# Kernel optimization log

Hardware: AMD Instinct MI355X
Metric: run time of the kernel (lower is better)

Reference implementation:

```python
import math
import jax, jax.numpy as jnp
import numpy as np

B, C, H, W = 8, 512, 32, 32
NUM_HEADS = 8
HEAD_DIM = C // NUM_HEADS


def setup_inputs() -> dict:
    key = jax.random.key(0)
    ks = jax.random.split(key, 5)
    scale = 1.0 / math.sqrt(C)
    return {
        "x": jax.random.normal(ks[0], (B, C, H, W), dtype=jnp.float32),
        "Wq": jax.random.normal(ks[1], (C, C), dtype=jnp.float32) * scale,
        "bq": jnp.zeros((C,), dtype=jnp.float32),
        "Wk": jax.random.normal(ks[2], (C, C), dtype=jnp.float32) * scale,
        "bk": jnp.zeros((C,), dtype=jnp.float32),
        "Wv": jax.random.normal(ks[3], (C, C), dtype=jnp.float32) * scale,
        "bv": jnp.zeros((C,), dtype=jnp.float32),
        "Wo": jax.random.normal(ks[4], (C, C), dtype=jnp.float32) * scale,
        "bo": jnp.zeros((C,), dtype=jnp.float32),
    }


def reference(x, Wq, bq, Wk, bk, Wv, bv, Wo, bo):
    b, c, h, w = x.shape
    t = h * w
    # (B,C,H,W) -> (B,T,C) token sequence
    xt = x.reshape(b, c, t).transpose(0, 2, 1)
    Q = xt @ Wq + bq
    K = xt @ Wk + bk
    V = xt @ Wv + bv
    # (B,T,C) -> (B,nh,T,hd)
    def split_heads(z):
        return z.reshape(b, t, NUM_HEADS, HEAD_DIM).transpose(0, 2, 1, 3)
    Qh, Kh, Vh = split_heads(Q), split_heads(K), split_heads(V)
    S = jnp.einsum("bhqd,bhkd->bhqk", Qh, Kh) / math.sqrt(HEAD_DIM)
    A = jax.nn.softmax(S, axis=-1)  # dropout p=0.0 -> identity
    Y = jnp.einsum("bhqk,bhkd->bhqd", A, Vh)
    Y = Y.transpose(0, 2, 1, 3).reshape(b, t, c)
    O = Y @ Wo + bo
    out = xt + O
    return out.transpose(0, 2, 1).reshape(b, c, h, w)
```

## Files before the change

### kernel.cpp

```cpp
#include <hip/hip_runtime.h>
#include <hip/hip_bf16.h>

#define B_  8
#define C_  512
#define T_  1024
#define NH_ 8
#define HD_ 64

using short8 = __attribute__((ext_vector_type(8))) short;
using f32x4  = __attribute__((ext_vector_type(4))) float;
using us4    = __attribute__((ext_vector_type(4))) unsigned short;
using u32x2  = __attribute__((ext_vector_type(2))) unsigned int;

__device__ __forceinline__ unsigned short f2bf(float f) {
    unsigned u = __builtin_bit_cast(unsigned, f);
    u += 0x7fff + ((u >> 16) & 1);
    return (unsigned short)(u >> 16);
}
__device__ __forceinline__ unsigned pack2bf(float lo, float hi) {
    __hip_bfloat162 h = __float22bfloat162_rn(float2{lo, hi});
    unsigned u;
    __builtin_memcpy(&u, &h, 4);
    return u;
}

__device__ __forceinline__ void gload_lds16(const ushort* g, ushort* l) {
    __builtin_amdgcn_global_load_lds(
        (const __attribute__((address_space(1))) void*)g,
        (__attribute__((address_space(3))) void*)l, 16, 0, 0);
}

__global__ __launch_bounds__(256) void k_transpose_x(const float* __restrict__ x,
                                                     ushort* __restrict__ xt) {
    __shared__ float tile[32][33];
    int b = blockIdx.z, t0 = blockIdx.x * 32, c0 = blockIdx.y * 32;
    int tx = threadIdx.x & 31, ty = threadIdx.x >> 5;
#pragma unroll
    for (int i = 0; i < 4; i++)
        tile[ty + i * 8][tx] = x[((size_t)b * C_ + c0 + ty + i * 8) * T_ + t0 + tx];
    __syncthreads();
#pragma unroll
    for (int i = 0; i < 4; i++)
        xt[((size_t)b * T_ + t0 + ty + i * 8) * C_ + c0 + tx] = f2bf(tile[tx][ty + i * 8]);
}

__global__ __launch_bounds__(256) void k_transpose_w(const float* __restrict__ Wq,
                                                     const float* __restrict__ Wk,
                                                     const float* __restrict__ Wv,
                                                     const float* __restrict__ Wo,
                                                     ushort* __restrict__ Wqkvt,
                                                     ushort* __restrict__ Wot) {
    __shared__ float tile[32][33];
    int m = blockIdx.z;
    const float* W = (m == 0) ? Wq : (m == 1) ? Wk : (m == 2) ? Wv : Wo;
    ushort* dst = (m < 3) ? (Wqkvt + (size_t)m * C_ * C_) : Wot;
    float scale = (m == 0) ? 0.125f : 1.0f;
    int k0 = blockIdx.x * 32, n0 = blockIdx.y * 32;
    int tx = threadIdx.x & 31, ty = threadIdx.x >> 5;
#pragma unroll
    for (int i = 0; i < 4; i++)
        tile[ty + i * 8][tx] = W[(size_t)(k0 + ty + i * 8) * C_ + n0 + tx];
    __syncthreads();
#pragma unroll
    for (int i = 0; i < 4; i++)
        dst[(size_t)(n0 + ty + i * 8) * C_ + k0 + tx] = f2bf(tile[tx][ty + i * 8] * scale);
}

__device__ __forceinline__ void gemm_core(const ushort* __restrict__ A,
                                          const ushort* __restrict__ Bt,
                                          int row0, int col0, int tid,
                                          ushort* As, ushort* Bs, f32x4 acc[4][4]) {
    f32x4 zero = {0.f, 0.f, 0.f, 0.f};
#pragma unroll
    for (int i = 0; i < 4; i++)
#pragma unroll
        for (int j = 0; j < 4; j++) acc[i][j] = zero;
    int lane = tid & 63, w = tid >> 6;
    int ql = lane & 15, g = lane >> 4;
    int wm = (w >> 1) * 64, wn = (w & 1) * 64;
    int srow = lane >> 3;
    int scol8 = (lane & 7) ^ (srow & 7);

    for (int k0 = 0; k0 < C_; k0 += 64) {
#pragma unroll
        for (int i = 0; i < 4; i++) {
            int c = w * 4 + i;
            int r = c * 8 + srow;
            gload_lds16(A + (size_t)(row0 + r) * C_ + k0 + scol8 * 8, As + c * 512);
            gload_lds16(Bt + (size_t)(col0 + r) * C_ + k0 + scol8 * 8, Bs + c * 512);
        }
        __syncthreads();
#pragma unroll
        for (int s = 0; s < 2; s++) {
            short8 a[4], b[4];
            int cs = ((4 * s + g) ^ (ql & 7)) * 8;
#pragma unroll
            for (int mt = 0; mt < 4; mt++)
                a[mt] = *(const short8*)(As + (wm + mt * 16 + ql) * 64 + cs);
#pragma unroll
            for (int nt = 0; nt < 4; nt++)
                b[nt] = *(const short8*)(Bs + (wn + nt * 16 + ql) * 64 + cs);
#pragma unroll
            for (int mt = 0; mt < 4; mt++)
#pragma unroll
                for (int nt = 0; nt < 4; nt++)
                    acc[mt][nt] = __builtin_amdgcn_mfma_f32_16x16x32_bf16(
                        a[mt], b[nt], acc[mt][nt], 0, 0, 0);
        }
        __syncthreads();
    }
}

__global__ __launch_bounds__(256) void k_qkv(const ushort* __restrict__ xt,
                                             const ushort* __restrict__ Wqkvt,
                                             const float* __restrict__ bq,
                                             const float* __restrict__ bk,
                                             const float* __restrict__ bv,
                                             ushort* __restrict__ Qh,
                                             ushort* __restrict__ Kh,
                                             ushort* __restrict__ Vt) {
    __shared__ __align__(16) ushort As[128 * 64];
    __shared__ __align__(16) ushort Bs[128 * 64];
    f32x4 acc[4][4];
    int tid = threadIdx.x;
    int row0 = blockIdx.x * 128, col0 = blockIdx.y * 128;
    gemm_core(xt, Wqkvt, row0, col0, tid, As, Bs, acc);
    int lane = tid & 63, w = tid >> 6;
    int wm = (w >> 1) * 64, wn = (w & 1) * 64;
    int which = col0 >> 9;
    const float* bias = (which == 0) ? bq : (which == 1) ? bk : bv;
    float bscale = (which == 0) ? 0.125f : 1.0f;
#pragma unroll
    for (int mt = 0; mt < 4; mt++) {
        int grow0 = row0 + wm + mt * 16 + ((lane >> 4) << 2);
        int b = grow0 >> 10, t = grow0 & 1023;
#pragma unroll
        for (int nt = 0; nt < 4; nt++) {
            int gcol = col0 + wn + nt * 16 + (lane & 15);
            int hc = gcol & 511;
            float bsv = bias[hc] * bscale;
            int h = hc >> 6, d = hc & 63;
            if (which == 2) {
                us4 pk;
#pragma unroll
                for (int r = 0; r < 4; r++) pk[r] = f2bf(acc[mt][nt][r] + bsv);
                *(us4*)(Vt + ((size_t)(b * NH_ + h) * HD_ + d) * T_ + t) = pk;
            } else {
                ushort* dst = (which == 0) ? Qh : Kh;
#pragma unroll
                for (int r = 0; r < 4; r++)
                    dst[((size_t)(b * NH_ + h) * T_ + t + r) * HD_ + d] =
                        f2bf(acc[mt][nt][r] + bsv);
            }
        }
    }
}

__global__ __launch_bounds__(512) void k_attn(const ushort* __restrict__ Qh,
                                              const ushort* __restrict__ Kh,
                                              const ushort* __restrict__ Vt,
                                              ushort* __restrict__ Y) {
    __shared__ __align__(16) ushort Ks[2][64 * 64];
    __shared__ __align__(16) ushort Vs[2][64 * 64];
    __shared__ __align__(16) ushort Pws[8][16 * 64];
    int tid = threadIdx.x, lane = tid & 63, w = tid >> 6;
    int g = lane >> 4, ql = lane & 15;
    int bh = blockIdx.x & 63, q0 = (blockIdx.x >> 6) * 128;
    int b = bh >> 3, h = bh & 7;
    ushort* Pw = Pws[w];
    int srow = lane >> 3;
    int scol8 = (lane & 7) ^ (srow & 7);
    const ushort* Kbase = Kh + (size_t)bh * T_ * HD_;
    const ushort* Vbase = Vt + (size_t)bh * HD_ * T_;

    short8 qa[2];
#pragma unroll
    for (int s = 0; s < 2; s++)
        qa[s] = *(const short8*)(Qh + ((size_t)bh * T_ + q0 + w * 16 + ql) * HD_ + s * 32 + g * 8);

    short8 ones;
    {
        short ov = (ql == 0) ? (short)0x3F80 : (short)0;
#pragma unroll
        for (int j = 0; j < 8; j++) ones[j] = ov;
    }

    f32x4 o[4], o5;
    f32x4 zero = {0.f, 0.f, 0.f, 0.f};
#pragma unroll
    for (int i = 0; i < 4; i++) o[i] = zero;
    o5 = zero;

    {
        int r = w * 8 + srow;
        gload_lds16(Kbase + (size_t)r * HD_ + scol8 * 8, Ks[0] + w * 512);
        gload_lds16(Vbase + (size_t)r * T_ + scol8 * 8, Vs[0] + w * 512);
    }
    __syncthreads();

    for (int t = 0; t < 16; t++) {
        int cur = t & 1;
        const ushort* Kc = Ks[cur];
        const ushort* Vc = Vs[cur];
        if (t < 15) {
            int kv0 = (t + 1) * 64;
            int r = w * 8 + srow;
            gload_lds16(Kbase + (size_t)(kv0 + r) * HD_ + scol8 * 8, Ks[cur ^ 1] + w * 512);
            gload_lds16(Vbase + (size_t)r * T_ + kv0 + scol8 * 8, Vs[cur ^ 1] + w * 512);
        }

        f32x4 sT[4];
#pragma unroll
        for (int nt = 0; nt < 4; nt++) sT[nt] = zero;
        __builtin_amdgcn_s_setprio(1);
#pragma unroll
        for (int s = 0; s < 2; s++) {
            int cs = ((4 * s + g) ^ (ql & 7)) * 8;
#pragma unroll
            for (int nt = 0; nt < 4; nt++) {
                short8 ka = *(const short8*)(Kc + (nt * 16 + ql) * 64 + cs);
                sT[nt] = __builtin_amdgcn_mfma_f32_16x16x32_bf16(ka, qa[s], sT[nt], 0, 0, 0);
            }
        }
        __builtin_amdgcn_s_setprio(0);

#pragma unroll
        for (int nt = 0; nt < 4; nt++) {
            u32x2 pk;
            pk[0] = pack2bf(__expf(sT[nt][0]), __expf(sT[nt][1]));
            pk[1] = pack2bf(__expf(sT[nt][2]), __expf(sT[nt][3]));
            int gr = (2 * nt + (g >> 1)) ^ (ql & 7);
            *(u32x2*)(Pw + ql * 64 + gr * 8 + (g & 1) * 4) = pk;
        }

        __builtin_amdgcn_s_setprio(1);
#pragma unroll
        for (int s = 0; s < 2; s++) {
            int cs = ((4 * s + g) ^ (ql & 7)) * 8;
            short8 pa = *(const short8*)(Pw + ql * 64 + cs);
#pragma unroll
            for (int dt = 0; dt < 4; dt++) {
                short8 vb = *(const short8*)(Vc + (dt * 16 + ql) * 64 + cs);
                o[dt] = __builtin_amdgcn_mfma_f32_16x16x32_bf16(pa, vb, o[dt], 0, 0, 0);
            }
            o5 = __builtin_amdgcn_mfma_f32_16x16x32_bf16(pa, ones, o5, 0, 0, 0);
        }
        __builtin_amdgcn_s_setprio(0);
        __syncthreads();
    }

    float li[4];
#pragma unroll
    for (int r = 0; r < 4; r++) li[r] = 1.0f / __shfl(o5[r], g * 16);
#pragma unroll
    for (int dt = 0; dt < 4; dt++)
#pragma unroll
        for (int r = 0; r < 4; r++) {
            int t = q0 + w * 16 + 4 * g + r;
            int c = h * HD_ + dt * 16 + ql;
            Y[((size_t)b * T_ + t) * C_ + c] = f2bf(o[dt][r] * li[r]);
        }
}

__global__ __launch_bounds__(256) void k_oproj(const ushort* __restrict__ Y,
                                               const ushort* __restrict__ Wot,
                                               const float* __restrict__ bo,
                                               const float* __restrict__ x,
                                               float* __restrict__ out) {
    __shared__ __align__(16) ushort As[128 * 64];
    __shared__ __align__(16) ushort Bs[128 * 64];
    f32x4 acc[4][4];
    int tid = threadIdx.x;
    int row0 = blockIdx.x * 128, col0 = blockIdx.y * 128;
    gemm_core(Y, Wot, row0, col0, tid, As, Bs, acc);
    int lane = tid & 63, w = tid >> 6;
    int wm = (w >> 1) * 64, wn = (w & 1) * 64;
#pragma unroll
    for (int mt = 0; mt < 4; mt++) {
        int grow0 = row0 + wm + mt * 16 + ((lane >> 4) << 2);
        int b = grow0 >> 10, t = grow0 & 1023;
#pragma unroll
        for (int nt = 0; nt < 4; nt++) {
            int c = col0 + wn + nt * 16 + (lane & 15);
            float bsv = bo[c];
            size_t off = ((size_t)b * C_ + c) * T_ + t;
            float4 xv = *(const float4*)(x + off);
            float4 ov;
            ov.x = acc[mt][nt][0] + xv.x + bsv;
            ov.y = acc[mt][nt][1] + xv.y + bsv;
            ov.z = acc[mt][nt][2] + xv.z + bsv;
            ov.w = acc[mt][nt][3] + xv.w + bsv;
            *(float4*)(out + off) = ov;
        }
    }
}

extern "C" void kernel_launch(void* const* d_in, const int* in_sizes, int n_in,
                              void* d_out, int out_size, void* d_ws, size_t ws_size,
                              hipStream_t stream) {
    const float* x  = (const float*)d_in[0];
    const float* Wq = (const float*)d_in[1];
    const float* bq = (const float*)d_in[2];
    const float* Wk = (const float*)d_in[3];
    const float* bk = (const float*)d_in[4];
    const float* Wv = (const float*)d_in[5];
    const float* bv = (const float*)d_in[6];
    const float* Wo = (const float*)d_in[7];
    const float* bo = (const float*)d_in[8];
    float* out = (float*)d_out;

    char* ws = (char*)d_ws;
    ushort* xt    = (ushort*)(ws + 0);
    ushort* Wqkvt = (ushort*)(ws + 8388608);
    ushort* Wot   = (ushort*)(ws + 9961472);
    ushort* Qh    = (ushort*)(ws + 10485760);
    ushort* Kh    = (ushort*)(ws + 18874368);
    ushort* Vt    = (ushort*)(ws + 27262976);
    ushort* Yw    = xt;

    k_transpose_x<<<dim3(32, 16, 8), 256, 0, stream>>>(x, xt);
    k_transpose_w<<<dim3(16, 16, 4), 256, 0, stream>>>(Wq, Wk, Wv, Wo, Wqkvt, Wot);
    k_qkv<<<dim3(64, 12), 256, 0, stream>>>(xt, Wqkvt, bq, bk, bv, Qh, Kh, Vt);
    k_attn<<<dim3(512), 512, 0, stream>>>(Qh, Kh, Vt, Yw);
    k_oproj<<<dim3(64, 4), 256, 0, stream>>>(Yw, Wot, bo, x, out);
}
```

Baseline: 83.43 us.

## Double-buffer GEMM LDS tiles and fold log2e into Q scale for exp2

The shared GEMM core now keeps two LDS buffers per operand and prefetches the next K tile while computing on the current one, so global loads overlap with MFMA work. It also raises wave priority during the MFMA section. Separately, the Q scale absorbs log2(e), so attention can call the hardware exp2 directly instead of __expf. The extra buffers double the LDS per block (64KB), which may reduce occupancy.

```diff
diff --git a/kernel.cpp b/kernel.cpp
--- a/kernel.cpp
+++ b/kernel.cpp
@@ -6,6 +6,8 @@
 #define T_  1024
 #define NH_ 8
 #define HD_ 64
+
+#define QSCALE 0.1803368801111243f
 
 using short8 = __attribute__((ext_vector_type(8))) short;
 using f32x4  = __attribute__((ext_vector_type(4))) float;
@@ -54,7 +56,7 @@
     int m = blockIdx.z;
     const float* W = (m == 0) ? Wq : (m == 1) ? Wk : (m == 2) ? Wv : Wo;
     ushort* dst = (m < 3) ? (Wqkvt + (size_t)m * C_ * C_) : Wot;
-    float scale = (m == 0) ? 0.125f : 1.0f;
+    float scale = (m == 0) ? QSCALE : 1.0f;
     int k0 = blockIdx.x * 32, n0 = blockIdx.y * 32;
     int tx = threadIdx.x & 31, ty = threadIdx.x >> 5;
 #pragma unroll
@@ -69,7 +71,8 @@
 __device__ __forceinline__ void gemm_core(const ushort* __restrict__ A,
                                           const ushort* __restrict__ Bt,
                                           int row0, int col0, int tid,
-                                          ushort* As, ushort* Bs, f32x4 acc[4][4]) {
+                                          ushort (*As)[8192], ushort (*Bs)[8192],
+                                          f32x4 acc[4][4]) {
     f32x4 zero = {0.f, 0.f, 0.f, 0.f};
 #pragma unroll
     for (int i = 0; i < 4; i++)
@@ -81,25 +84,40 @@
     int srow = lane >> 3;
     int scol8 = (lane & 7) ^ (srow & 7);
 
-    for (int k0 = 0; k0 < C_; k0 += 64) {
-#pragma unroll
-        for (int i = 0; i < 4; i++) {
-            int c = w * 4 + i;
-            int r = c * 8 + srow;
-            gload_lds16(A + (size_t)(row0 + r) * C_ + k0 + scol8 * 8, As + c * 512);
-            gload_lds16(Bt + (size_t)(col0 + r) * C_ + k0 + scol8 * 8, Bs + c * 512);
-        }
-        __syncthreads();
+#pragma unroll
+    for (int i = 0; i < 4; i++) {
+        int c = w * 4 + i;
+        int r = c * 8 + srow;
+        gload_lds16(A + (size_t)(row0 + r) * C_ + scol8 * 8, As[0] + c * 512);
+        gload_lds16(Bt + (size_t)(col0 + r) * C_ + scol8 * 8, Bs[0] + c * 512);
+    }
+    __syncthreads();
+
+    for (int kt = 0; kt < 8; kt++) {
+        int cur = kt & 1;
+        if (kt < 7) {
+            int k0 = (kt + 1) * 64;
+#pragma unroll
+            for (int i = 0; i < 4; i++) {
+                int c = w * 4 + i;
+                int r = c * 8 + srow;
+                gload_lds16(A + (size_t)(row0 + r) * C_ + k0 + scol8 * 8, As[cur ^ 1] + c * 512);
+                gload_lds16(Bt + (size_t)(col0 + r) * C_ + k0 + scol8 * 8, Bs[cur ^ 1] + c * 512);
+            }
+        }
+        const ushort* Ac = As[cur];
+        const ushort* Bc = Bs[cur];
+        __builtin_amdgcn_s_setprio(1);
 #pragma unroll
         for (int s = 0; s < 2; s++) {
             short8 a[4], b[4];
             int cs = ((4 * s + g) ^ (ql & 7)) * 8;
 #pragma unroll
             for (int mt = 0; mt < 4; mt++)
-                a[mt] = *(const short8*)(As + (wm + mt * 16 + ql) * 64 + cs);
+                a[mt] = *(const short8*)(Ac + (wm + mt * 16 + ql) * 64 + cs);
 #pragma unroll
             for (int nt = 0; nt < 4; nt++)
-                b[nt] = *(const short8*)(Bs + (wn + nt * 16 + ql) * 64 + cs);
+                b[nt] = *(const short8*)(Bc + (wn + nt * 16 + ql) * 64 + cs);
 #pragma unroll
             for (int mt = 0; mt < 4; mt++)
 #pragma unroll
@@ -107,6 +125,7 @@
                     acc[mt][nt] = __builtin_amdgcn_mfma_f32_16x16x32_bf16(
                         a[mt], b[nt], acc[mt][nt], 0, 0, 0);
         }
+        __builtin_amdgcn_s_setprio(0);
         __syncthreads();
     }
 }
@@ -119,8 +138,8 @@
                                              ushort* __restrict__ Qh,
                                              ushort* __restrict__ Kh,
                                              ushort* __restrict__ Vt) {
-    __shared__ __align__(16) ushort As[128 * 64];
-    __shared__ __align__(16) ushort Bs[128 * 64];
+    __shared__ __align__(16) ushort As[2][8192];
+    __shared__ __align__(16) ushort Bs[2][8192];
     f32x4 acc[4][4];
     int tid = threadIdx.x;
     int row0 = blockIdx.x * 128, col0 = blockIdx.y * 128;
@@ -129,7 +148,7 @@
     int wm = (w >> 1) * 64, wn = (w & 1) * 64;
     int which = col0 >> 9;
     const float* bias = (which == 0) ? bq : (which == 1) ? bk : bv;
-    float bscale = (which == 0) ? 0.125f : 1.0f;
+    float bscale = (which == 0) ? QSCALE : 1.0f;
 #pragma unroll
     for (int mt = 0; mt < 4; mt++) {
         int grow0 = row0 + wm + mt * 16 + ((lane >> 4) << 2);
@@ -227,8 +246,8 @@
 #pragma unroll
         for (int nt = 0; nt < 4; nt++) {
             u32x2 pk;
-            pk[0] = pack2bf(__expf(sT[nt][0]), __expf(sT[nt][1]));
-            pk[1] = pack2bf(__expf(sT[nt][2]), __expf(sT[nt][3]));
+            pk[0] = pack2bf(__builtin_amdgcn_exp2f(sT[nt][0]), __builtin_amdgcn_exp2f(sT[nt][1]));
+            pk[1] = pack2bf(__builtin_amdgcn_exp2f(sT[nt][2]), __builtin_amdgcn_exp2f(sT[nt][3]));
             int gr = (2 * nt + (g >> 1)) ^ (ql & 7);
             *(u32x2*)(Pw + ql * 64 + gr * 8 + (g & 1) * 4) = pk;
         }
@@ -267,8 +286,8 @@
                                                const float* __restrict__ bo,
                                                const float* __restrict__ x,
                                                float* __restrict__ out) {
-    __shared__ __align__(16) ushort As[128 * 64];
-    __shared__ __align__(16) ushort Bs[128 * 64];
+    __shared__ __align__(16) ushort As[2][8192];
+    __shared__ __align__(16) ushort Bs[2][8192];
     f32x4 acc[4][4];
     int tid = threadIdx.x;
     int row0 = blockIdx.x * 128, col0 = blockIdx.y * 128;
```

After: 79.38 us. -4.9%, faster.
